# Kernel tuning notes

Hardware: AMD Instinct MI355X
Metric: run time of the kernel (lower is better)

The kernel has to match this reference:

```python
import jax, jax.numpy as jnp
import numpy as np
import math

B, S, D, H = 4, 1024, 1024, 16
HD = D // H  # head_size = 64
NEG = -1e9


def setup_inputs() -> dict:
    rng = jax.random.key(0)
    ks = jax.random.split(rng, 12)
    f = lambda k, shape: jax.random.normal(k, shape, dtype=jnp.float32)
    inp = {
        "query": f(ks[0], (B, S, D)),
        "key": f(ks[1], (B, S, D)),
        "value": f(ks[2], (B, S, D)),
        # rel: correlation matrix between interactions, non-negative
        "rel": jax.random.uniform(ks[3], (B, S, S), dtype=jnp.float32),
        "l1": jnp.float32(0.5),
        "l2": jnp.float32(0.5),
        # timestamp: |t_i - t_j| time gaps
        "timestamp": jax.random.uniform(ks[4], (B, S, S), dtype=jnp.float32) * 10.0,
        "encode_pos": 0,
        "pos_key_embeds": f(ks[5], (32, HD)) * 0.02,
        "pos_value_embeds": f(ks[6], (32, HD)) * 0.02,
        # causal mask: True = disallowed (future) position
        "mask": jnp.broadcast_to(jnp.triu(jnp.ones((S, S), dtype=bool), k=1), (B, S, S)),
        "Wq": f(ks[7], (D, D)) / math.sqrt(D), "bq": jnp.zeros((D,), jnp.float32),
        "Wk": f(ks[8], (D, D)) / math.sqrt(D), "bk": jnp.zeros((D,), jnp.float32),
        "Wv": f(ks[9], (D, D)) / math.sqrt(D), "bv": jnp.zeros((D,), jnp.float32),
    }
    return inp


def _split_heads(x, W, b):
    # nn.Linear uses x @ W.T + b ; reshape to [B,H,S,HD]
    y = x @ W.T + b
    return y.reshape(B, S, H, HD).transpose(0, 2, 1, 3)


def reference(query, key, value, rel, l1, l2, timestamp, encode_pos,
              pos_key_embeds, pos_value_embeds, mask,
              Wq, bq, Wk, bk, Wv, bv):
    assert encode_pos == 0, "reference implements the encode_pos=False path"
    q = _split_heads(query, Wq, bq)   # [B,H,S,HD]
    k = _split_heads(key, Wk, bk)
    v = _split_heads(value, Wv, bv)

    m = mask[:, None]  # [B,1,S,S], True = masked

    # relation-based attention: future-mask rel, softmax over nonzero entries
    relm = rel[:, None] * (~m).astype(jnp.float32)          # [B,1,S,S]
    rel_attn = jax.nn.softmax(jnp.where(relm == 0, -1e5, relm), axis=-1)

    # scaled dot-product scores
    scores = jnp.einsum("bhqd,bhkd->bhqk", q, k) / jnp.sqrt(jnp.float32(HD))
    scores = jnp.where(m, NEG, scores)
    prob_attn = jax.nn.softmax(scores, axis=-1)             # [B,H,S,S]

    # time-decay attention: exp(-|dt|), future-masked
    ts = jnp.exp(-jnp.abs(timestamp))[:, None]              # [B,1,S,S]
    ts = jnp.where(m, NEG, ts)
    time_attn = jax.nn.softmax(ts, axis=-1)

    prob = (1.0 - l2) * prob_attn + l2 * time_attn
    prob = (1.0 - l1) * prob + l1 * rel_attn                # [B,H,S,S]

    out = jnp.einsum("bhqk,bhkd->bhqd", prob, v)
    out = out.transpose(0, 2, 1, 3).reshape(B, S, D)
    return out, prob
```

## Files before the change

### kernel.cpp

```cpp
#include <hip/hip_runtime.h>
#include <cstdint>
#include <cstddef>


typedef __bf16 bf16_t;
typedef __bf16 bf16x8 __attribute__((ext_vector_type(8)));
typedef __bf16 bf16x4 __attribute__((ext_vector_type(4)));
typedef float  f32x4  __attribute__((ext_vector_type(4)));

__device__ __forceinline__ f32x4 mfma16(bf16x8 a, bf16x8 b, f32x4 c) {
  return __builtin_amdgcn_mfma_f32_16x16x32_bf16(a, b, c, 0, 0, 0);
}

__device__ __forceinline__ void g2l16(const void* g, void* l) {
  __builtin_amdgcn_global_load_lds((__attribute__((address_space(1))) void*)(g),
                                   (__attribute__((address_space(3))) void*)(l),
                                   16, 0, 0);
}

__global__ __launch_bounds__(256) void cast_kernel(
    const float* __restrict__ q, const float* __restrict__ k, const float* __restrict__ v,
    const float* __restrict__ wq, const float* __restrict__ wk, const float* __restrict__ wv,
    bf16_t* __restrict__ Xb, bf16_t* __restrict__ Wb) {
  int i = blockIdx.x * 256 + threadIdx.x;
  const float* src;
  bf16_t* dst;
  if (i < 3145728) {
    int m = i >> 20;
    size_t o = (size_t)(i & 1048575) * 4;
    src = (m == 0) ? q : (m == 1) ? k : v;
    dst = Xb + (size_t)m * 4194304 + o;
    src += o;
  } else {
    int j = i - 3145728;
    int m = j >> 18;
    size_t o = (size_t)(j & 262143) * 4;
    src = (m == 0) ? wq : (m == 1) ? wk : wv;
    dst = Wb + (size_t)m * 1048576 + o;
    src += o;
  }
  f32x4 f = *(const f32x4*)src;
  bf16x4 r;
  r[0] = (bf16_t)f[0]; r[1] = (bf16_t)f[1]; r[2] = (bf16_t)f[2]; r[3] = (bf16_t)f[3];
  *(bf16x4*)dst = r;
}

__global__ __launch_bounds__(256) void gemm_qkv(
    const bf16_t* __restrict__ Xb, const bf16_t* __restrict__ Wb,
    const float* __restrict__ bqp, const float* __restrict__ bkp, const float* __restrict__ bvp,
    bf16_t* __restrict__ Yb) {
  __shared__ __align__(16) bf16_t As[128 * 32];
  __shared__ __align__(16) bf16_t Bs[128 * 32];
  const int z = blockIdx.z;
  const bf16_t* X = Xb + (size_t)z * 4194304;
  const bf16_t* W = Wb + (size_t)z * 1048576;
  const float* bias = (z == 0) ? bqp : (z == 1) ? bkp : bvp;
  bf16_t* Y = Yb + (size_t)z * 4194304;

  const int tid = threadIdx.x;
  const int lane = tid & 63;
  const int w = tid >> 6;
  const int wr = w >> 1, wc = w & 1;
  const int rb = blockIdx.y * 128, cb = blockIdx.x * 128;
  const int lr = lane & 15, g = lane >> 4;

  f32x4 zero = {0.f, 0.f, 0.f, 0.f};
  f32x4 acc[4][4];
  for (int m = 0; m < 4; ++m)
    for (int n = 0; n < 4; ++n) acc[m][n] = zero;

  for (int k0 = 0; k0 < 1024; k0 += 32) {
    for (int r = 0; r < 2; ++r) {
      int cid = r * 256 + tid;
      int row = cid >> 2;
      int ko = (cid & 3) * 8;
      const bf16_t* ga = X + ((size_t)(rb + row) * 1024 + k0 + ko);
      const bf16_t* gb = W + ((size_t)(cb + row) * 1024 + k0 + ko);
      char* la = (char*)As + r * 4096 + w * 1024;
      char* lb = (char*)Bs + r * 4096 + w * 1024;
      g2l16(ga, la);
      g2l16(gb, lb);
    }
    asm volatile("s_waitcnt vmcnt(0)" ::: "memory");
    __syncthreads();

    bf16x8 afr[4], bfr[4];
    for (int m = 0; m < 4; ++m)
      afr[m] = *(const bf16x8*)&As[(wr * 64 + m * 16 + lr) * 32 + g * 8];
    for (int n = 0; n < 4; ++n)
      bfr[n] = *(const bf16x8*)&Bs[(wc * 64 + n * 16 + lr) * 32 + g * 8];
    for (int m = 0; m < 4; ++m)
      for (int n = 0; n < 4; ++n)
        acc[m][n] = mfma16(afr[m], bfr[n], acc[m][n]);
    __syncthreads();
  }

  for (int m = 0; m < 4; ++m) {
    int rowb = rb + wr * 64 + m * 16 + g * 4;
    for (int n = 0; n < 4; ++n) {
      int col = cb + wc * 64 + n * 16 + lr;
      float bb = bias[col];
      for (int r = 0; r < 4; ++r)
        Y[(size_t)(rowb + r) * 1024 + col] = (bf16_t)(acc[m][n][r] + bb);
    }
  }
}

__global__ __launch_bounds__(256) void transpose_v(const bf16_t* __restrict__ Yv,
                                                   bf16_t* __restrict__ vT) {
  __shared__ __align__(16) bf16_t t[64][68];
  const int bh = blockIdx.y, b = bh >> 4, h = bh & 15;
  const int s0 = blockIdx.x * 64;
  const int tid = threadIdx.x;
  for (int i = 0; i < 4; ++i) {
    int c = tid + i * 256;
    int r = c >> 4, c4 = (c & 15) * 4;
    bf16x4 v4 = *(const bf16x4*)(Yv + ((size_t)(b * 1024 + s0 + r)) * 1024 + h * 64 + c4);
    *(bf16x4*)&t[r][c4] = v4;
  }
  __syncthreads();
  for (int i = 0; i < 4; ++i) {
    int c = tid + i * 256;
    int hd = c >> 4, s4 = (c & 15) * 4;
    bf16x4 o;
    o[0] = t[s4 + 0][hd]; o[1] = t[s4 + 1][hd];
    o[2] = t[s4 + 2][hd]; o[3] = t[s4 + 3][hd];
    *(bf16x4*)(vT + ((size_t)(bh * 64 + hd)) * 1024 + s0 + s4) = o;
  }
}

__global__ __launch_bounds__(256) void base_kernel(
    const float* __restrict__ rel, const float* __restrict__ ts,
    const float* __restrict__ l1p, const float* __restrict__ l2p,
    bf16_t* __restrict__ baseb) {
  const int row = blockIdx.x;
  const int q = row & 1023;
  const int tid = threadIdx.x;
  const int w = tid >> 6;
  const float l1 = *l1p, l2 = *l2p;
  const float cr = l1, ct = (1.f - l1) * l2;

  f32x4 rv = *(const f32x4*)(rel + (size_t)row * 1024 + tid * 4);
  f32x4 tv = *(const f32x4*)(ts  + (size_t)row * 1024 + tid * 4);

  float x[4], t[4];
  for (int j = 0; j < 4; ++j) {
    int k = tid * 4 + j;
    bool msk = k > q;
    float rj = rv[j];
    x[j] = (msk || rj == 0.f) ? -100000.f : rj;
    t[j] = msk ? -1e9f : __expf(-fabsf(tv[j]));
  }
  float mr = fmaxf(fmaxf(x[0], x[1]), fmaxf(x[2], x[3]));
  float mt = fmaxf(fmaxf(t[0], t[1]), fmaxf(t[2], t[3]));
  for (int o = 1; o < 64; o <<= 1) {
    mr = fmaxf(mr, __shfl_xor(mr, o));
    mt = fmaxf(mt, __shfl_xor(mt, o));
  }
  __shared__ float red[4][4];
  if ((tid & 63) == 0) { red[0][w] = mr; red[1][w] = mt; }
  __syncthreads();
  mr = fmaxf(fmaxf(red[0][0], red[0][1]), fmaxf(red[0][2], red[0][3]));
  mt = fmaxf(fmaxf(red[1][0], red[1][1]), fmaxf(red[1][2], red[1][3]));

  float er[4], et[4], sr = 0.f, st = 0.f;
  for (int j = 0; j < 4; ++j) {
    er[j] = __expf(x[j] - mr);
    et[j] = __expf(t[j] - mt);
    sr += er[j]; st += et[j];
  }
  for (int o = 1; o < 64; o <<= 1) {
    sr += __shfl_xor(sr, o);
    st += __shfl_xor(st, o);
  }
  if ((tid & 63) == 0) { red[2][w] = sr; red[3][w] = st; }
  __syncthreads();
  sr = red[2][0] + red[2][1] + red[2][2] + red[2][3];
  st = red[3][0] + red[3][1] + red[3][2] + red[3][3];

  float isr = cr / sr, ist = ct / st;
  bf16x4 o4;
  for (int j = 0; j < 4; ++j) o4[j] = (bf16_t)(er[j] * isr + et[j] * ist);
  *(bf16x4*)(baseb + (size_t)row * 1024 + tid * 4) = o4;
}

__global__ __launch_bounds__(256) void attn_kernel(
    const bf16_t* __restrict__ qY, const bf16_t* __restrict__ kY,
    const bf16_t* __restrict__ vT, const bf16_t* __restrict__ baseb,
    const float* __restrict__ l1p, const float* __restrict__ l2p,
    float* __restrict__ outp, float* __restrict__ probp) {
  const int bh = blockIdx.x, b = bh >> 4, h = bh & 15;
  const int qg = 63 - blockIdx.y;
  const int q0 = qg * 16;
  const int tid = threadIdx.x, lane = tid & 63, w = tid >> 6;
  const int lr = lane & 15, g = lane >> 4;
  const int qr = q0 + lr;
  const float l1 = *l1p, l2 = *l2p;
  const float c1 = (1.f - l1) * (1.f - l2);

  __shared__ __align__(16) union ShMem {
    bf16_t plds[4][16][36];
    float  pvred[4][16][64];
  } sh;
  __shared__ float zred[4][16];

  const bf16_t* qbase = qY + ((size_t)(b * 1024 + q0 + lr)) * 1024 + h * 64 + g * 8;
  bf16x8 bq0 = *(const bf16x8*)qbase;
  bf16x8 bq1 = *(const bf16x8*)(qbase + 32);

  const bf16_t* kptr = kY + ((size_t)(b * 1024 + lr)) * 1024 + h * 64 + g * 8;

  const int nch = q0 / 32 + 1;
  f32x4 zero = {0.f, 0.f, 0.f, 0.f};

  bf16x4 esave[8][2];
  float zp = 0.f;
#pragma unroll
  for (int c = 0; c < 8; ++c) {
    const int ch = w + 4 * c;
    if (ch < nch) {
      const bf16_t* p0 = kptr + (size_t)ch * 32768;
      bf16x8 k0 = *(const bf16x8*)p0;
      bf16x8 k1 = *(const bf16x8*)(p0 + 32);
      bf16x8 k2 = *(const bf16x8*)(p0 + 16384);
      bf16x8 k3 = *(const bf16x8*)(p0 + 16416);
      f32x4 s0 = zero, s1 = zero;
      s0 = mfma16(k0, bq0, s0);
      s0 = mfma16(k1, bq1, s0);
      s1 = mfma16(k2, bq0, s1);
      s1 = mfma16(k3, bq1, s1);
      const int kc0 = ch * 32 + g * 4;
      bf16x4 e0, e1;
      for (int r = 0; r < 4; ++r) {
        float ea = (kc0 + r > qr) ? 0.f : __expf(s0[r] * 0.125f);
        float eb = (kc0 + 16 + r > qr) ? 0.f : __expf(s1[r] * 0.125f);
        zp += ea + eb;
        e0[r] = (bf16_t)ea;
        e1[r] = (bf16_t)eb;
      }
      esave[c][0] = e0;
      esave[c][1] = e1;
    }
  }
  zp += __shfl_xor(zp, 16);
  zp += __shfl_xor(zp, 32);
  if (lane < 16) zred[w][lr] = zp;
  __syncthreads();
  const float Z = zred[0][lr] + zred[1][lr] + zred[2][lr] + zred[3][lr];
  const float invz = c1 / Z;

  const bf16_t* baserow = baseb + ((size_t)(b * 1024 + qr)) * 1024;
  float* probrow = probp + ((size_t)(bh * 1024 + qr)) * 1024;
  const bf16_t* vbase = vT + ((size_t)(bh * 64 + lr)) * 1024 + g * 8;

  f32x4 acc[4];
  for (int cf = 0; cf < 4; ++cf) acc[cf] = zero;

#pragma unroll
  for (int c = 0; c < 8; ++c) {
    const int ch = w + 4 * c;
    if (ch < nch) {
      bf16x8 vv[4];
      for (int cf = 0; cf < 4; ++cf)
        vv[cf] = *(const bf16x8*)(vbase + (size_t)cf * 16384 + ch * 32);
      for (int f = 0; f < 2; ++f) {
        const int kc0 = ch * 32 + f * 16 + g * 4;
        bf16x4 b4 = *(const bf16x4*)(baserow + kc0);
        bf16x4 eb = esave[c][f];
        f32x4 p;
        bf16x4 pb;
        for (int r = 0; r < 4; ++r) {
          p[r] = (float)eb[r] * invz + (float)b4[r];
          pb[r] = (bf16_t)p[r];
        }
        __builtin_nontemporal_store(p, (f32x4*)(probrow + kc0));
        *(bf16x4*)&sh.plds[w][lr][f * 16 + g * 4] = pb;
      }
      asm volatile("s_waitcnt lgkmcnt(0)" ::: "memory");
      bf16x8 pa = *(const bf16x8*)&sh.plds[w][lr][g * 8];
      for (int cf = 0; cf < 4; ++cf)
        acc[cf] = mfma16(pa, vv[cf], acc[cf]);
    }
  }

  const int kstart = nch * 32;
  for (int i = 0; i < 4; ++i) {
    int qrr = q0 + w * 4 + i;
    const bf16_t* brow = baseb + ((size_t)(b * 1024 + qrr)) * 1024;
    float* prow = probp + ((size_t)(bh * 1024 + qrr)) * 1024;
    for (int k = kstart + lane * 4; k < 1024; k += 256) {
      bf16x4 b4 = *(const bf16x4*)(brow + k);
      f32x4 f4;
      f4[0] = (float)b4[0]; f4[1] = (float)b4[1];
      f4[2] = (float)b4[2]; f4[3] = (float)b4[3];
      __builtin_nontemporal_store(f4, (f32x4*)(prow + k));
    }
  }

  __syncthreads();
  for (int cf = 0; cf < 4; ++cf)
    for (int r = 0; r < 4; ++r)
      sh.pvred[w][g * 4 + r][cf * 16 + lr] = acc[cf][r];
  __syncthreads();
  {
    const int row0 = tid >> 6, hd = tid & 63;
    for (int i = 0; i < 4; ++i) {
      int row = row0 + 4 * i;
      float s = sh.pvred[0][row][hd] + sh.pvred[1][row][hd] +
                sh.pvred[2][row][hd] + sh.pvred[3][row][hd];
      outp[((size_t)(b * 1024 + q0 + row)) * 1024 + h * 64 + hd] = s;
    }
  }
}

extern "C" void kernel_launch(void* const* d_in, const int* in_sizes, int n_in,
                              void* d_out, int out_size, void* d_ws, size_t ws_size,
                              hipStream_t stream) {
  const float* query = (const float*)d_in[0];
  const float* key   = (const float*)d_in[1];
  const float* value = (const float*)d_in[2];
  const float* rel   = (const float*)d_in[3];
  const float* l1p   = (const float*)d_in[4];
  const float* l2p   = (const float*)d_in[5];
  const float* tsp   = (const float*)d_in[6];
  const float* Wq = (const float*)d_in[11];
  const float* bq = (const float*)d_in[12];
  const float* Wk = (const float*)d_in[13];
  const float* bk = (const float*)d_in[14];
  const float* Wv = (const float*)d_in[15];
  const float* bv = (const float*)d_in[16];

  char* ws = (char*)d_ws;
  bf16_t* Xb    = (bf16_t*)(ws);
  bf16_t* Wb    = (bf16_t*)(ws + 25165824);
  bf16_t* Yb    = (bf16_t*)(ws + 31457280);
  bf16_t* vT    = (bf16_t*)(ws + 56623104);
  bf16_t* baseb = (bf16_t*)(ws + 65011712);

  float* outp  = (float*)d_out;
  float* probp = outp + 4194304;

  cast_kernel<<<dim3(15360), dim3(256), 0, stream>>>(query, key, value, Wq, Wk, Wv, Xb, Wb);
  gemm_qkv<<<dim3(8, 32, 3), dim3(256), 0, stream>>>(Xb, Wb, bq, bk, bv, Yb);
  transpose_v<<<dim3(16, 64), dim3(256), 0, stream>>>(Yb + (size_t)2 * 4194304, vT);
  base_kernel<<<dim3(4096), dim3(256), 0, stream>>>(rel, tsp, l1p, l2p, baseb);
  attn_kernel<<<dim3(64, 64), dim3(256), 0, stream>>>(Yb, Yb + 4194304, vT, baseb,
                                                      l1p, l2p, outp, probp);
}
```

Measured before the change: 175.1 us.

## Stage prob tiles through LDS for coalesced stores, move masked tail to separate kernel

The attention kernel now writes the fp32 probability tile into LDS and re-reads it in a row-contiguous layout, so each wave issues coalesced 128-byte-row nontemporal stores instead of strided 16-byte stores per lane. The bf16 MFMA operand is rebuilt from the same fp32 LDS buffer. The upper-triangle tail that copies base probabilities for masked positions moves out of attn_kernel into a separate tail_kernel launched afterwards, which removes load imbalance in the attention blocks. The cost is an extra launch and larger LDS use. Replacing the lgkmcnt wait with a plain compiler barrier may leave an LDS ordering hazard within the wave.

Result: slower. 193.7 us (+10.6%).

```diff
diff --git a/kernel.cpp b/kernel.cpp
--- a/kernel.cpp
+++ b/kernel.cpp
@@ -184,6 +184,27 @@
   *(bf16x4*)(baseb + (size_t)row * 1024 + tid * 4) = o4;
 }
 
+__global__ __launch_bounds__(256) void tail_kernel(
+    const bf16_t* __restrict__ baseb, float* __restrict__ probp) {
+  const int bh = blockIdx.x, b = bh >> 4;
+  const int qg = blockIdx.y;
+  const int kstart = (qg / 2 + 1) * 32;
+  if (kstart >= 1024) return;
+  const int q0 = qg * 16;
+  const int tid = threadIdx.x;
+  for (int r = 0; r < 16; ++r) {
+    const bf16_t* brow = baseb + ((size_t)(b * 1024 + q0 + r)) * 1024;
+    float* prow = probp + ((size_t)(bh * 1024 + q0 + r)) * 1024;
+    for (int k = kstart + tid * 4; k < 1024; k += 1024) {
+      bf16x4 b4 = *(const bf16x4*)(brow + k);
+      f32x4 f4;
+      f4[0] = (float)b4[0]; f4[1] = (float)b4[1];
+      f4[2] = (float)b4[2]; f4[3] = (float)b4[3];
+      __builtin_nontemporal_store(f4, (f32x4*)(prow + k));
+    }
+  }
+}
+
 __global__ __launch_bounds__(256) void attn_kernel(
     const bf16_t* __restrict__ qY, const bf16_t* __restrict__ kY,
     const bf16_t* __restrict__ vT, const bf16_t* __restrict__ baseb,
@@ -199,8 +220,8 @@
   const float c1 = (1.f - l1) * (1.f - l2);
 
   __shared__ __align__(16) union ShMem {
-    bf16_t plds[4][16][36];
-    float  pvred[4][16][64];
+    float pf[4][16][40];
+    float pvred[4][16][64];
   } sh;
   __shared__ float zred[4][16];
 
@@ -250,8 +271,9 @@
   const float invz = c1 / Z;
 
   const bf16_t* baserow = baseb + ((size_t)(b * 1024 + qr)) * 1024;
-  float* probrow = probp + ((size_t)(bh * 1024 + qr)) * 1024;
   const bf16_t* vbase = vT + ((size_t)(bh * 64 + lr)) * 1024 + g * 8;
+  float* probbase = probp + ((size_t)(bh * 1024 + q0)) * 1024;
+  const int srow = lane >> 3, scol = (lane & 7) * 4;
 
   f32x4 acc[4];
   for (int cf = 0; cf < 4; ++cf) acc[cf] = zero;
@@ -268,32 +290,26 @@
         bf16x4 b4 = *(const bf16x4*)(baserow + kc0);
         bf16x4 eb = esave[c][f];
         f32x4 p;
-        bf16x4 pb;
-        for (int r = 0; r < 4; ++r) {
+        for (int r = 0; r < 4; ++r)
           p[r] = (float)eb[r] * invz + (float)b4[r];
-          pb[r] = (bf16_t)p[r];
-        }
-        __builtin_nontemporal_store(p, (f32x4*)(probrow + kc0));
-        *(bf16x4*)&sh.plds[w][lr][f * 16 + g * 4] = pb;
+        *(f32x4*)&sh.pf[w][lr][f * 16 + g * 4] = p;
       }
-      asm volatile("s_waitcnt lgkmcnt(0)" ::: "memory");
-      bf16x8 pa = *(const bf16x8*)&sh.plds[w][lr][g * 8];
+      asm volatile("" ::: "memory");
+      f32x4 p0 = *(const f32x4*)&sh.pf[w][srow][scol];
+      f32x4 p1 = *(const f32x4*)&sh.pf[w][srow + 8][scol];
+      float* pr = probbase + (size_t)srow * 1024 + ch * 32 + scol;
+      __builtin_nontemporal_store(p0, (f32x4*)pr);
+      __builtin_nontemporal_store(p1, (f32x4*)(pr + 8 * 1024));
+      f32x4 fa0 = *(const f32x4*)&sh.pf[w][lr][g * 8];
+      f32x4 fa1 = *(const f32x4*)&sh.pf[w][lr][g * 8 + 4];
+      bf16x8 pa;
+      for (int j = 0; j < 4; ++j) {
+        pa[j] = (bf16_t)fa0[j];
+        pa[4 + j] = (bf16_t)fa1[j];
+      }
       for (int cf = 0; cf < 4; ++cf)
         acc[cf] = mfma16(pa, vv[cf], acc[cf]);
-    }
-  }
-
-  const int kstart = nch * 32;
-  for (int i = 0; i < 4; ++i) {
-    int qrr = q0 + w * 4 + i;
-    const bf16_t* brow = baseb + ((size_t)(b * 1024 + qrr)) * 1024;
-    float* prow = probp + ((size_t)(bh * 1024 + qrr)) * 1024;
-    for (int k = kstart + lane * 4; k < 1024; k += 256) {
-      bf16x4 b4 = *(const bf16x4*)(brow + k);
-      f32x4 f4;
-      f4[0] = (float)b4[0]; f4[1] = (float)b4[1];
-      f4[2] = (float)b4[2]; f4[3] = (float)b4[3];
-      __builtin_nontemporal_store(f4, (f32x4*)(prow + k));
+      asm volatile("" ::: "memory");
     }
   }
 
@@ -346,4 +362,5 @@
   base_kernel<<<dim3(4096), dim3(256), 0, stream>>>(rel, tsp, l1p, l2p, baseb);
   attn_kernel<<<dim3(64, 64), dim3(256), 0, stream>>>(Yb, Yb + 4194304, vT, baseb,
                                                       l1p, l2p, outp, probp);
-}
+  tail_kernel<<<dim3(64, 64), dim3(256), 0, stream>>>(baseb, probp);
+}
```
